# Performance work log

Measured on AMD Instinct MI355X. Metric: run time of the kernel, lower is better.

## Reference

```python
import jax, jax.numpy as jnp
import numpy as np
import math

B, C, S, O, K = 64, 271, 512, 512, 32  # seq_len S must equal out_channels O (einsum constraint in original)

def setup_inputs() -> dict:
    key = jax.random.key(0)
    k1, k2, k3, k4, k5 = jax.random.split(key, 5)
    x = jax.random.normal(k1, (B, C, S), dtype=jnp.float32)
    fourier_features = jax.random.normal(k2, (O, K, K, 4), dtype=jnp.float32)
    sensor_positions = jax.random.uniform(k3, (C, 2), dtype=jnp.float32)
    proj_w = jax.random.normal(k4, (O, C), dtype=jnp.float32) / np.float32(math.sqrt(C))
    proj_b = jax.random.normal(k5, (O,), dtype=jnp.float32) * 0.02
    return {"x": x, "fourier_features": fourier_features,
            "sensor_positions": sensor_positions, "proj_w": proj_w, "proj_b": proj_b}

def reference(x, fourier_features, sensor_positions, proj_w, proj_b):
    Kdim = fourier_features.shape[1]
    freqs = 2.0 * jnp.pi * jnp.arange(Kdim, dtype=jnp.float32) / Kdim
    # meshgrid(freqs_x, freqs_y, indexing='ij') stacked on last dim -> [K,K,2]
    grid = jnp.stack(jnp.meshgrid(freqs, freqs, indexing='ij'), axis=-1)
    # feature map is batch-independent: [C,K,K,2] -> sin/cos cat -> [C,K,K,4]
    fm = sensor_positions[:, None, None, :] * grid[None]
    fm = jnp.concatenate([jnp.sin(fm), jnp.cos(fm)], axis=-1)
    # attention logits [O,C]; original expands over batch but result is identical per batch
    att = jnp.einsum('ckhw,okhw->oc', fm, fourier_features)
    att = jax.nn.softmax(att, axis=0)  # softmax over out_channels (dim=1 of [B,O,C])
    # 1x1 Conv1d: [B,C,S] -> [B,O,S]
    xp = jnp.einsum('bcs,oc->bos', x, proj_w) + proj_b[None, :, None]
    # original: einsum('bci,bio->bco', xp[B,O,S], attn[B,O,C]); contraction over S(==O)
    out = jnp.einsum('bps,sq->bpq', xp, att)  # [B,O,C]
    return out
```

## Files before the change

kernel.cpp:

```cpp
#include <hip/hip_runtime.h>
#include <hip/hip_bf16.h>
#include <math.h>


typedef short s16x8 __attribute__((ext_vector_type(8)));
typedef short s16x4 __attribute__((ext_vector_type(4)));
typedef float f32x4 __attribute__((ext_vector_type(4)));

#define GLOBAL_AS __attribute__((address_space(1)))
#define LDS_AS    __attribute__((address_space(3)))

__device__ __forceinline__ short f2bf(float f) {
    __hip_bfloat16 h = __float2bfloat16(f);
    return *reinterpret_cast<short*>(&h);
}

#define Cdim 271
#define CpK  288
#define Sdim 512
#define Odim 512
#define MF   17344
#define MFp  17408

template<int MODE, int SWAP>
__global__ __launch_bounds__(512) void gemm_bf16(
    const short* __restrict__ A, int lda,
    const short* __restrict__ BT, int ldb,
    int nk,
    void* __restrict__ OutV,
    const float* __restrict__ bias)
{
    const int m0 = (SWAP ? blockIdx.x : blockIdx.y) * 128;
    const int n0 = (SWAP ? blockIdx.y : blockIdx.x) * 128;

    __shared__ short As[4][128 * 32];
    __shared__ short Bs[4][128 * 32];

    const int t = threadIdx.x;
    const int lane = t & 63;
    const int wid = t >> 6;
    const int wr = wid >> 2;
    const int wc = wid & 3;
    const int lr = lane & 15, lkq = lane >> 4;

    f32x4 acc[4][2];
    #pragma unroll
    for (int i = 0; i < 4; ++i)
        #pragma unroll
        for (int j = 0; j < 2; ++j)
            acc[i][j] = (f32x4){0.f, 0.f, 0.f, 0.f};

    const int srow = wid * 16 + (lane >> 2);
    const int skk  = (((lane & 3) ^ ((lane >> 3) & 3)) * 8);
    const short* pA = A + (long)(m0 + srow) * lda + skk;
    const short* pB = BT + (long)(n0 + srow) * ldb + skk;
    const int ldsOff = wid * 512;

    const int kxs = ((lkq ^ ((lr >> 1) & 3)) << 3);
    const int aBase = (wr * 64 + lr) * 32 + kxs;
    const int bBase = (wc * 32 + lr) * 32 + kxs;

    auto stage = [&](int buf, int kt) {
        const int k0 = kt * 32;
        __builtin_amdgcn_global_load_lds((const GLOBAL_AS void*)(pA + k0),
            (LDS_AS void*)&As[buf][ldsOff], 16, 0, 0);
        __builtin_amdgcn_global_load_lds((const GLOBAL_AS void*)(pB + k0),
            (LDS_AS void*)&Bs[buf][ldsOff], 16, 0, 0);
    };

    auto compute = [&](int buf) {
        s16x8 af[4], bfv[2];
        #pragma unroll
        for (int m = 0; m < 4; ++m)
            af[m] = *(const s16x8*)&As[buf][aBase + m * 512];
        #pragma unroll
        for (int n = 0; n < 2; ++n)
            bfv[n] = *(const s16x8*)&Bs[buf][bBase + n * 512];
        #pragma unroll
        for (int m = 0; m < 4; ++m)
            #pragma unroll
            for (int n = 0; n < 2; ++n)
                acc[m][n] = __builtin_amdgcn_mfma_f32_16x16x32_bf16(af[m], bfv[n], acc[m][n], 0, 0, 0);
    };

    stage(0, 0); stage(1, 1); stage(2, 2);
    for (int kt = 0; kt < nk; ++kt) {
        const int rem = nk - 1 - kt;
        if (rem >= 2)      asm volatile("s_waitcnt vmcnt(4)" ::: "memory");
        else if (rem == 1) asm volatile("s_waitcnt vmcnt(2)" ::: "memory");
        else               asm volatile("s_waitcnt vmcnt(0)" ::: "memory");
        __builtin_amdgcn_s_barrier();
        __builtin_amdgcn_sched_barrier(0);
        if (kt + 3 < nk) stage((kt + 3) & 3, kt + 3);
        compute(kt & 3);
    }

    if (MODE == 0) {
        short* Oy = (short*)OutV;
        #pragma unroll
        for (int i = 0; i < 4; ++i) {
            const int gmb = m0 + wr * 64 + i * 16 + lkq * 4;
            if (gmb >= MF) continue;
            const int b0 = gmb / Cdim;
            const int c0 = gmb - b0 * Cdim;
            const bool whole = (c0 + 3 < Cdim);
            #pragma unroll
            for (int j = 0; j < 2; ++j) {
                const int gn = n0 + wc * 32 + j * 16 + lr;
                if (gn >= Cdim) continue;
                if (whole) {
                    s16x4 v;
                    #pragma unroll
                    for (int r = 0; r < 4; ++r) v[r] = f2bf(acc[i][j][r]);
                    *(s16x4*)&Oy[((long)b0 * Cdim + gn) * CpK + c0] = v;
                } else {
                    #pragma unroll
                    for (int r = 0; r < 4; ++r) {
                        const int gm = gmb + r;
                        const int bb = gm / Cdim;
                        const int cc = gm - bb * Cdim;
                        Oy[((long)bb * Cdim + gn) * CpK + cc] = f2bf(acc[i][j][r]);
                    }
                }
            }
        }
    } else {
        float* O = (float*)OutV;
        #pragma unroll
        for (int j = 0; j < 2; ++j) {
            const int gn = n0 + wc * 32 + j * 16 + lr;
            if (gn >= MF) continue;
            const int b = gn / Cdim;
            const int q = gn - b * Cdim;
            float* ob = O + (long)b * Odim * Cdim + q;
            #pragma unroll
            for (int i = 0; i < 4; ++i) {
                const int gmb = m0 + wr * 64 + i * 16 + lkq * 4;
                #pragma unroll
                for (int r = 0; r < 4; ++r) {
                    const int gm = gmb + r;
                    ob[(long)gm * Cdim] = acc[i][j][r] + bias[gm];
                }
            }
        }
    }
}

#define CONVX_BLOCKS 4352
#define PW_BLOCKS    576
#define FF_BLOCKS    256

__global__ __launch_bounds__(256) void prep(
    const float* __restrict__ x,  short* __restrict__ xb,
    const float* __restrict__ pw, short* __restrict__ pwb,
    const float* __restrict__ ff, float* __restrict__ GT)
{
    const int blk = blockIdx.x;
    const int t = threadIdx.x;

    if (blk < CONVX_BLOCKS) {
        const long i8 = ((long)blk * 256 + t) * 8;
        s16x8 v = {0, 0, 0, 0, 0, 0, 0, 0};
        if (i8 < (long)MF * Sdim) {
            const f32x4 u0 = *(const f32x4*)&x[i8];
            const f32x4 u1 = *(const f32x4*)&x[i8 + 4];
            #pragma unroll
            for (int j = 0; j < 4; ++j) { v[j] = f2bf(u0[j]); v[4 + j] = f2bf(u1[j]); }
        }
        *(s16x8*)&xb[i8] = v;
        return;
    }
    if (blk < CONVX_BLOCKS + PW_BLOCKS) {
        const int idx = (blk - CONVX_BLOCKS) * 256 + t;
        const int p = idx / CpK;
        const int k = idx - p * CpK;
        pwb[idx] = (k < Cdim) ? f2bf(pw[(long)p * Cdim + k]) : (short)0;
        return;
    }
    __shared__ float L[2][32 * 132];
    const int fb = blk - (CONVX_BLOCKS + PW_BLOCKS);
    const int half = t >> 7;
    const int tl = t & 127;
    const int o = fb * 2 + half;
    const float* base = ff + (long)o * 4096;
    #pragma unroll
    for (int ch = 0; ch < 8; ++ch) {
        const int g = ch * 512 + tl * 4;
        const f32x4 v = *(const f32x4*)&base[g];
        *(f32x4*)&L[half][(g >> 7) * 132 + (g & 127)] = v;
    }
    __syncthreads();
    const int gq = tl >> 5, idx = tl & 31;
    float s = 0.f;
    if (gq == 0 || gq == 2) {
        const int w = (gq == 0) ? 0 : 2;
        #pragma unroll 8
        for (int j = 0; j < 32; ++j) s += L[half][idx * 132 + j * 4 + w];
    } else {
        const int w = (gq == 1) ? 1 : 3;
        #pragma unroll 8
        for (int i = 0; i < 32; ++i) s += L[half][i * 132 + idx * 4 + w];
    }
    GT[tl * 512 + o] = s;
}

__device__ __forceinline__ float wave_max(float v) {
    #pragma unroll
    for (int off = 32; off; off >>= 1) v = fmaxf(v, __shfl_xor(v, off));
    return v;
}
__device__ __forceinline__ float wave_sum(float v) {
    #pragma unroll
    for (int off = 32; off; off >>= 1) v += __shfl_xor(v, off);
    return v;
}

__global__ __launch_bounds__(256) void att_fused(
    const float* __restrict__ GT,
    const float* __restrict__ sp,
    short* __restrict__ attT)
{
    const int c = blockIdx.x;
    const int t = threadIdx.x;
    short* row = attT + (long)c * Sdim;
    if (c >= Cdim) {
        row[t] = 0; row[t + 256] = 0;
        return;
    }
    __shared__ float u[128];
    __shared__ float red[4];
    if (t < 128) {
        const int g = t >> 5, k = t & 31;
        const float f = 6.283185307179586477f * (float)k / 32.0f;
        const float p = sp[c * 2 + (g & 1)];
        const float ang = p * f;
        u[t] = (g < 2) ? sinf(ang) : cosf(ang);
    }
    __syncthreads();

    float l0 = 0.f, l1 = 0.f;
    #pragma unroll 8
    for (int k = 0; k < 128; ++k) {
        const float uk = u[k];
        l0 = fmaf(GT[k * 512 + t], uk, l0);
        l1 = fmaf(GT[k * 512 + t + 256], uk, l1);
    }

    const int lane = t & 63, wid = t >> 6;
    float m = wave_max(fmaxf(l0, l1));
    if (lane == 0) red[wid] = m;
    __syncthreads();
    m = fmaxf(fmaxf(red[0], red[1]), fmaxf(red[2], red[3]));
    const float e0 = expf(l0 - m), e1 = expf(l1 - m);
    float s = wave_sum(e0 + e1);
    __syncthreads();
    if (lane == 0) red[wid] = s;
    __syncthreads();
    s = red[0] + red[1] + red[2] + red[3];
    const float inv = 1.f / s;
    row[t]       = f2bf(e0 * inv);
    row[t + 256] = f2bf(e1 * inv);
}

extern "C" void kernel_launch(void* const* d_in, const int* in_sizes, int n_in,
                              void* d_out, int out_size, void* d_ws, size_t ws_size,
                              hipStream_t stream)
{
    const float* x  = (const float*)d_in[0];
    const float* ff = (const float*)d_in[1];
    const float* sp = (const float*)d_in[2];
    const float* pw = (const float*)d_in[3];
    const float* pb = (const float*)d_in[4];
    float* out = (float*)d_out;

    const int S = Sdim, O = Odim;

    float* ws   = (float*)d_ws;
    float* GT   = ws;
    short* xb   = (short*)(GT + 128 * 512);
    short* attT = xb + (long)MFp * S;
    short* pwb  = attT + 384L * S;
    short* yT   = pwb + (long)O * CpK;

    prep<<<CONVX_BLOCKS + PW_BLOCKS + FF_BLOCKS, 256, 0, stream>>>(
        x, xb, pw, pwb, ff, GT);

    att_fused<<<384, 256, 0, stream>>>(GT, sp, attT);

    gemm_bf16<0, 1><<<dim3(MFp / 128, 3), 512, 0, stream>>>(
        xb, S, attT, S, S / 32, (void*)yT, nullptr);

    gemm_bf16<1, 0><<<dim3(MFp / 128, O / 128), 512, 0, stream>>>(
        pwb, CpK, yT, CpK, CpK / 32, (void*)out, pb);
}
```

Before: 67.01 us.

## Use 3-stage LDS pipeline, raise occupancy, stage MODE0 epilogue through LDS

Shrinks the LDS ring from four stages to three, kept in one shared pool, and adds a launch-bounds occupancy hint of six so more blocks can be resident per CU. The MODE 0 epilogue now transposes the bf16 tile through LDS and writes 16-byte vectors along the contiguous dimension, replacing scattered 8-byte stores. The cost is one fewer stage of prefetch to hide load latency, plus two extra barriers and LDS traffic in the epilogue.

```diff
diff --git a/kernel.cpp b/kernel.cpp
--- a/kernel.cpp
+++ b/kernel.cpp
@@ -23,7 +23,7 @@
 #define MFp  17408
 
 template<int MODE, int SWAP>
-__global__ __launch_bounds__(512) void gemm_bf16(
+__global__ __launch_bounds__(512, 6) void gemm_bf16(
     const short* __restrict__ A, int lda,
     const short* __restrict__ BT, int ldb,
     int nk,
@@ -33,8 +33,7 @@
     const int m0 = (SWAP ? blockIdx.x : blockIdx.y) * 128;
     const int n0 = (SWAP ? blockIdx.y : blockIdx.x) * 128;
 
-    __shared__ short As[4][128 * 32];
-    __shared__ short Bs[4][128 * 32];
+    __shared__ short pool[24576];
 
     const int t = threadIdx.x;
     const int lane = t & 63;
@@ -63,19 +62,19 @@
     auto stage = [&](int buf, int kt) {
         const int k0 = kt * 32;
         __builtin_amdgcn_global_load_lds((const GLOBAL_AS void*)(pA + k0),
-            (LDS_AS void*)&As[buf][ldsOff], 16, 0, 0);
+            (LDS_AS void*)&pool[buf * 4096 + ldsOff], 16, 0, 0);
         __builtin_amdgcn_global_load_lds((const GLOBAL_AS void*)(pB + k0),
-            (LDS_AS void*)&Bs[buf][ldsOff], 16, 0, 0);
+            (LDS_AS void*)&pool[12288 + buf * 4096 + ldsOff], 16, 0, 0);
     };
 
     auto compute = [&](int buf) {
         s16x8 af[4], bfv[2];
         #pragma unroll
         for (int m = 0; m < 4; ++m)
-            af[m] = *(const s16x8*)&As[buf][aBase + m * 512];
+            af[m] = *(const s16x8*)&pool[buf * 4096 + aBase + m * 512];
         #pragma unroll
         for (int n = 0; n < 2; ++n)
-            bfv[n] = *(const s16x8*)&Bs[buf][bBase + n * 512];
+            bfv[n] = *(const s16x8*)&pool[12288 + buf * 4096 + bBase + n * 512];
         #pragma unroll
         for (int m = 0; m < 4; ++m)
             #pragma unroll
@@ -83,43 +82,57 @@
                 acc[m][n] = __builtin_amdgcn_mfma_f32_16x16x32_bf16(af[m], bfv[n], acc[m][n], 0, 0, 0);
     };
 
-    stage(0, 0); stage(1, 1); stage(2, 2);
+    stage(0, 0); stage(1, 1);
+    int bc = 0, bs = 2;
     for (int kt = 0; kt < nk; ++kt) {
-        const int rem = nk - 1 - kt;
-        if (rem >= 2)      asm volatile("s_waitcnt vmcnt(4)" ::: "memory");
-        else if (rem == 1) asm volatile("s_waitcnt vmcnt(2)" ::: "memory");
-        else               asm volatile("s_waitcnt vmcnt(0)" ::: "memory");
+        if (kt + 1 < nk) asm volatile("s_waitcnt vmcnt(2)" ::: "memory");
+        else             asm volatile("s_waitcnt vmcnt(0)" ::: "memory");
         __builtin_amdgcn_s_barrier();
         __builtin_amdgcn_sched_barrier(0);
-        if (kt + 3 < nk) stage((kt + 3) & 3, kt + 3);
-        compute(kt & 3);
+        if (kt + 2 < nk) stage(bs, kt + 2);
+        compute(bc);
+        bc = (bc == 2) ? 0 : bc + 1;
+        bs = (bs == 2) ? 0 : bs + 1;
     }
 
     if (MODE == 0) {
-        short* Oy = (short*)OutV;
+        __syncthreads();
+        short* T = pool;
         #pragma unroll
         for (int i = 0; i < 4; ++i) {
-            const int gmb = m0 + wr * 64 + i * 16 + lkq * 4;
-            if (gmb >= MF) continue;
-            const int b0 = gmb / Cdim;
-            const int c0 = gmb - b0 * Cdim;
-            const bool whole = (c0 + 3 < Cdim);
+            const int ml = wr * 64 + i * 16 + lkq * 4;
             #pragma unroll
             for (int j = 0; j < 2; ++j) {
-                const int gn = n0 + wc * 32 + j * 16 + lr;
-                if (gn >= Cdim) continue;
-                if (whole) {
-                    s16x4 v;
-                    #pragma unroll
-                    for (int r = 0; r < 4; ++r) v[r] = f2bf(acc[i][j][r]);
-                    *(s16x4*)&Oy[((long)b0 * Cdim + gn) * CpK + c0] = v;
+                const int ql = wc * 32 + j * 16 + lr;
+                s16x4 v;
+                #pragma unroll
+                for (int r = 0; r < 4; ++r) v[r] = f2bf(acc[i][j][r]);
+                *(s16x4*)&T[ql * 132 + ml] = v;
+            }
+        }
+        __syncthreads();
+        short* Oy = (short*)OutV;
+        #pragma unroll
+        for (int p = 0; p < 4; ++p) {
+            const int ql = p * 32 + (t >> 4);
+            const int gq = n0 + ql;
+            const int mlc = (t & 15) * 8;
+            const s16x8 v = *(const s16x8*)&T[ql * 132 + mlc];
+            const int gm0 = m0 + mlc;
+            if (gq < Cdim && gm0 < MF) {
+                const int b0 = gm0 / Cdim;
+                const int c0 = gm0 - b0 * Cdim;
+                if (c0 + 8 <= Cdim) {
+                    *(s16x8*)&Oy[((long)b0 * Cdim + gq) * CpK + c0] = v;
                 } else {
                     #pragma unroll
-                    for (int r = 0; r < 4; ++r) {
-                        const int gm = gmb + r;
-                        const int bb = gm / Cdim;
-                        const int cc = gm - bb * Cdim;
-                        Oy[((long)bb * Cdim + gn) * CpK + cc] = f2bf(acc[i][j][r]);
+                    for (int r = 0; r < 8; ++r) {
+                        const int gm = gm0 + r;
+                        if (gm < MF) {
+                            const int bb = gm / Cdim;
+                            const int cc = gm - bb * Cdim;
+                            Oy[((long)bb * Cdim + gq) * CpK + cc] = v[r];
+                        }
                     }
                 }
             }
```

After: 60.99 us. 9.0% less time.
